# Kernel optimization log

Hardware: AMD Instinct MI355X
Metric: run time of the kernel (lower is better)

## Reference

```python
import jax, jax.numpy as jnp
import numpy as np

N = 100000
E = 800000
D = 128


def setup_inputs() -> dict:
    key = jax.random.key(0)
    k1, k2, k3, k4 = jax.random.split(key, 4)
    x = jax.random.normal(k1, (N, D), dtype=jnp.float32)
    edge_index = jax.random.randint(k2, (2, E), 0, N, dtype=jnp.int64)
    s = 1.0 / np.sqrt(D)
    W1 = jax.random.uniform(k3, (D, D), jnp.float32, -s, s)
    b1 = jnp.zeros((D,), jnp.float32)
    W2 = jax.random.uniform(k4, (D, D), jnp.float32, -s, s)
    b2 = jnp.zeros((D,), jnp.float32)
    return {"x": x, "edge_index": edge_index, "W1": W1, "b1": b1, "W2": W2, "b2": b2}


def _degree(idx, n, dtype):
    return jax.ops.segment_sum(jnp.ones(idx.shape, dtype), idx, num_segments=n)


def _graph_conv(x, row, col, W, b, residual, act):
    n = x.shape[0]
    deg_out = jnp.clip(_degree(row, n, x.dtype), 1.0)          # [N]
    x_src = x * jax.lax.rsqrt(deg_out)[:, None]                # [N, D]
    # scatter-add messages from source (row) into target (col)
    agg = jax.ops.segment_sum(x_src[row], col, num_segments=n)  # [N, D]
    out = agg @ W.T + b
    deg_in = jnp.clip(_degree(col, n, x.dtype), 1.0)
    out = out * jax.lax.rsqrt(deg_in)[:, None]
    if residual:
        out = out + x  # res_fc is Identity (in_dim == out_dim)
    if act:
        out = jax.nn.relu(out)
    return out


def reference(x, edge_index, W1, b1, W2, b2):
    row, col = edge_index[0], edge_index[1]
    # layer 1: relu + residual; layer 2 (last, encoding=False): no act, no residual
    h = _graph_conv(x, row, col, W1, b1, residual=True, act=True)
    h = _graph_conv(h, row, col, W2, b2, residual=False, act=False)
    return h
```

## Files before the change

kernel.cpp:

```cpp
#include <hip/hip_runtime.h>


#define NN 100000
#define EE 800000
#define DD 128
#define NB1 98
#define NTILE (NN / 16)

#define CC 64
#define CH (EE / CC)
#define HALF 50000
#define HWORDS 12500
#define NWORDS 25000

typedef __attribute__((ext_vector_type(8))) short short8;
typedef __attribute__((ext_vector_type(4))) float floatx4;

__device__ inline float bf2f(unsigned int u16) {
    union { unsigned int i; float f; } c;
    c.i = u16 << 16;
    return c.f;
}
__device__ inline ushort f2bf(float f) {
    union { float f; unsigned int i; } c;
    c.f = f;
    unsigned int u = c.i;
    return (ushort)((u + 0x7fffu + ((u >> 16) & 1u)) >> 16);
}

__global__ __launch_bounds__(512) void count_kernel(const int* __restrict__ row,
                                                    const int* __restrict__ col,
                                                    unsigned int* __restrict__ partial_out,
                                                    unsigned int* __restrict__ partial_in,
                                                    unsigned char* __restrict__ off_u8) {
    __shared__ unsigned int h[HWORDS];
    for (int i = threadIdx.x; i < HWORDS; i += 512) h[i] = 0;
    __syncthreads();

    const int kind = blockIdx.x >> 7;
    const int r = (blockIdx.x >> 6) & 1;
    const int c = blockIdx.x & 63;
    const int* __restrict__ idx = kind ? row : col;
    const int base = c * CH;
    const int lo = r * HALF;

    for (int t = threadIdx.x; t < CH; t += 512) {
        const int e = base + t;
        const unsigned int d = (unsigned int)(idx[e] - lo);
        if (d < (unsigned int)HALF) {
            const int sh = 8 * (d & 3);
            unsigned int old = atomicAdd(&h[d >> 2], 1u << sh);
            if (kind == 0) off_u8[e] = (unsigned char)((old >> sh) & 0xffu);
        }
    }
    __syncthreads();

    unsigned int* dst = (kind ? partial_out : partial_in) + c * NWORDS + r * HWORDS;
    for (int i = threadIdx.x; i < HWORDS; i += 512) dst[i] = h[i];
}

__global__ __launch_bounds__(256) void node_kernel(const unsigned int* __restrict__ partial_out,
                                                   const unsigned int* __restrict__ partial_in,
                                                   int* __restrict__ cnt_total,
                                                   unsigned int* __restrict__ xoff,
                                                   float* __restrict__ dinv_out,
                                                   float* __restrict__ dinv_in) {
    const int w = blockIdx.x * 256 + threadIdx.x;
    if (w >= NWORDS) return;
    unsigned int prefix = 0;
    unsigned int tot_out = 0;
#pragma unroll
    for (int c = 0; c < CC; ++c) {
        unsigned int v = partial_in[c * NWORDS + w];
        xoff[c * NWORDS + w] = prefix;
        prefix += v;
        tot_out += partial_out[c * NWORDS + w];
    }
    int4 ct;
    float4 fi, fo;
#pragma unroll
    for (int j = 0; j < 4; ++j) {
        int din  = (int)((prefix  >> (8 * j)) & 0xffu);
        int dout = (int)((tot_out >> (8 * j)) & 0xffu);
        ((int*)&ct)[j]   = din;
        ((float*)&fi)[j] = rsqrtf((float)max(din, 1));
        ((float*)&fo)[j] = rsqrtf((float)max(dout, 1));
    }
    ((int4*)cnt_total)[w] = ct;
    ((float4*)dinv_in)[w] = fi;
    ((float4*)dinv_out)[w] = fo;
}

__global__ __launch_bounds__(256) void scan1_kernel(const int* __restrict__ cnt,
                                                    int* __restrict__ excl,
                                                    int* __restrict__ bsums) {
    __shared__ int tmp[256];
    const int t = threadIdx.x;
    const int base = blockIdx.x * 1024 + t * 4;
    int a[4];
#pragma unroll
    for (int q = 0; q < 4; ++q) a[q] = (base + q < NN) ? cnt[base + q] : 0;
    int s = a[0] + a[1] + a[2] + a[3];
    tmp[t] = s;
    __syncthreads();
    for (int off = 1; off < 256; off <<= 1) {
        int v = 0;
        if (t >= off) v = tmp[t - off];
        __syncthreads();
        tmp[t] += v;
        __syncthreads();
    }
    int excl_s = tmp[t] - s;
    if (t == 255) bsums[blockIdx.x] = tmp[t];
    int run = excl_s;
#pragma unroll
    for (int q = 0; q < 4; ++q) {
        if (base + q < NN) excl[base + q] = run;
        run += a[q];
    }
}

__global__ __launch_bounds__(256) void scan2_kernel(int* __restrict__ bsums, int nb) {
    __shared__ int tmp[256];
    const int t = threadIdx.x;
    int s = (t < nb) ? bsums[t] : 0;
    tmp[t] = s;
    __syncthreads();
    for (int off = 1; off < 256; off <<= 1) {
        int v = 0;
        if (t >= off) v = tmp[t - off];
        __syncthreads();
        tmp[t] += v;
        __syncthreads();
    }
    if (t < nb) bsums[t] = tmp[t] - s;
}

__global__ __launch_bounds__(256) void scan3_kernel(const int* __restrict__ excl,
                                                    const int* __restrict__ bsums,
                                                    int* __restrict__ row_start) {
    int i = blockIdx.x * 256 + threadIdx.x;
    if (i < NN) row_start[i] = excl[i] + bsums[i >> 10];
}

__global__ __launch_bounds__(256) void fill_kernel(const int* __restrict__ row,
                                                   const int* __restrict__ col,
                                                   const int* __restrict__ row_start,
                                                   const unsigned char* __restrict__ xoff_u8,
                                                   const unsigned char* __restrict__ off_u8,
                                                   int* __restrict__ srcs) {
    int e = blockIdx.x * 256 + threadIdx.x;
    if (e < EE) {
        const int cl = col[e];
        const int c = e / CH;
        const int pos = row_start[cl] + (int)xoff_u8[(size_t)c * NN + cl] + (int)off_u8[e];
        srcs[pos] = row[e];
    }
}

__global__ __launch_bounds__(256) void prescale_kernel(const float* __restrict__ x,
                                                       const float* __restrict__ dinv_out,
                                                       ushort* __restrict__ xb) {
    int idx = blockIdx.x * 256 + threadIdx.x;
    if (idx >= NN * 32) return;
    int n = idx >> 5;
    float s = dinv_out[n];
    float4 v = ((const float4*)x)[idx];
    ushort4 o;
    o.x = f2bf(v.x * s);
    o.y = f2bf(v.y * s);
    o.z = f2bf(v.z * s);
    o.w = f2bf(v.w * s);
    ((ushort4*)xb)[idx] = o;
}

__global__ __launch_bounds__(256) void gather_kernel(const ushort* __restrict__ src,
                                                     const int* __restrict__ row_start,
                                                     const int* __restrict__ srcs,
                                                     ushort* __restrict__ agg) {
    const int node = blockIdx.x * 16 + (threadIdx.x >> 4);
    const int lane = threadIdx.x & 15;
    if (node >= NN) return;
    int p = row_start[node];
    const int end = (node + 1 < NN) ? row_start[node + 1] : EE;
    float a0 = 0.f, a1 = 0.f, a2 = 0.f, a3 = 0.f;
    float a4 = 0.f, a5 = 0.f, a6 = 0.f, a7 = 0.f;

#define ACCUM(V)                                     \
    do {                                             \
        a0 += bf2f((V).x & 0xffffu);                 \
        a1 += bf2f((V).x >> 16);                     \
        a2 += bf2f((V).y & 0xffffu);                 \
        a3 += bf2f((V).y >> 16);                     \
        a4 += bf2f((V).z & 0xffffu);                 \
        a5 += bf2f((V).z >> 16);                     \
        a6 += bf2f((V).w & 0xffffu);                 \
        a7 += bf2f((V).w >> 16);                     \
    } while (0)

    for (; p + 3 < end; p += 4) {
        int s0 = srcs[p];
        int s1 = srcs[p + 1];
        int s2 = srcs[p + 2];
        int s3 = srcs[p + 3];
        uint4 v0 = ((const uint4*)(src + (size_t)s0 * DD))[lane];
        uint4 v1 = ((const uint4*)(src + (size_t)s1 * DD))[lane];
        uint4 v2 = ((const uint4*)(src + (size_t)s2 * DD))[lane];
        uint4 v3 = ((const uint4*)(src + (size_t)s3 * DD))[lane];
        ACCUM(v0); ACCUM(v1); ACCUM(v2); ACCUM(v3);
    }
    for (; p < end; ++p) {
        int s0 = srcs[p];
        uint4 v0 = ((const uint4*)(src + (size_t)s0 * DD))[lane];
        ACCUM(v0);
    }
#undef ACCUM

    uint4 o;
    o.x = (unsigned int)f2bf(a0) | ((unsigned int)f2bf(a1) << 16);
    o.y = (unsigned int)f2bf(a2) | ((unsigned int)f2bf(a3) << 16);
    o.z = (unsigned int)f2bf(a4) | ((unsigned int)f2bf(a5) << 16);
    o.w = (unsigned int)f2bf(a6) | ((unsigned int)f2bf(a7) << 16);
    ((uint4*)(agg + (size_t)node * DD))[lane] = o;
}

template <bool L1>
__global__ __launch_bounds__(256) void gemm_ep(const ushort* __restrict__ agg,
                                               const float* __restrict__ W,
                                               const float* __restrict__ bias,
                                               const float* __restrict__ dinv_in,
                                               const float* __restrict__ dinv_out,
                                               const float* __restrict__ x,
                                               ushort* __restrict__ hs,
                                               float* __restrict__ out) {
    __shared__ ushort Ws[128 * 136];
    {
        int j = threadIdx.x >> 1;
        int k0 = (threadIdx.x & 1) * 64;
        const float4* wp = (const float4*)(W + (size_t)j * DD + k0);
        ushort* dst = Ws + j * 136 + k0;
#pragma unroll
        for (int q = 0; q < 16; ++q) {
            float4 v = wp[q];
            ushort4 o;
            o.x = f2bf(v.x); o.y = f2bf(v.y); o.z = f2bf(v.z); o.w = f2bf(v.w);
            *(ushort4*)(dst + q * 4) = o;
        }
    }
    __syncthreads();

    const int wave = threadIdx.x >> 6;
    const int lane = threadIdx.x & 63;
    const int tile = blockIdx.x * 4 + wave;
    if (tile >= NTILE) return;
    const int mi = lane & 15;
    const int quad = lane >> 4;
    const int m0 = tile * 16;

    floatx4 acc[8];
#pragma unroll
    for (int t = 0; t < 8; ++t) acc[t] = (floatx4){0.f, 0.f, 0.f, 0.f};

    const ushort* ap = agg + (size_t)(m0 + mi) * DD + quad * 8;
#pragma unroll
    for (int s = 0; s < 4; ++s) {
        short8 a = *(const short8*)(ap + s * 32);
#pragma unroll
        for (int t = 0; t < 8; ++t) {
            short8 b = *(const short8*)(Ws + (t * 16 + mi) * 136 + s * 32 + quad * 8);
            acc[t] = __builtin_amdgcn_mfma_f32_16x16x32_bf16(a, b, acc[t], 0, 0, 0);
        }
    }

    float dv[4], dov[4];
#pragma unroll
    for (int i = 0; i < 4; ++i) {
        int r = m0 + quad * 4 + i;
        dv[i] = dinv_in[r];
        if (L1) dov[i] = dinv_out[r];
    }
#pragma unroll
    for (int t = 0; t < 8; ++t) {
        int c = t * 16 + mi;
        float bv = bias[c];
#pragma unroll
        for (int i = 0; i < 4; ++i) {
            int r = m0 + quad * 4 + i;
            float o = (acc[t][i] + bv) * dv[i];
            if (L1) {
                o += x[(size_t)r * DD + c];
                o = fmaxf(o, 0.f);
                hs[(size_t)r * DD + c] = f2bf(o * dov[i]);
            } else {
                out[(size_t)r * DD + c] = o;
            }
        }
    }
}

extern "C" void kernel_launch(void* const* d_in, const int* in_sizes, int n_in,
                              void* d_out, int out_size, void* d_ws, size_t ws_size,
                              hipStream_t stream) {
    const float* x  = (const float*)d_in[0];
    const int*   ei = (const int*)d_in[1];
    const float* W1 = (const float*)d_in[2];
    const float* b1 = (const float*)d_in[3];
    const float* W2 = (const float*)d_in[4];
    const float* b2 = (const float*)d_in[5];
    float* out = (float*)d_out;

    const int* row = ei;
    const int* col = ei + EE;

    ushort* agg     = (ushort*)d_ws;
    ushort* xb      = agg + (size_t)NN * DD;
    float* dinv_out = (float*)(xb + (size_t)NN * DD);
    float* dinv_in  = dinv_out + NN;
    int*   cnt      = (int*)(dinv_in + NN);
    int*   excl     = cnt + NN;
    int*   row_st   = excl + NN;
    int*   srcs     = row_st + NN;
    int*   bsums    = srcs + EE;

    unsigned char* off_u8      = (unsigned char*)agg;
    unsigned int*  partial_in  = (unsigned int*)(off_u8 + EE);
    unsigned int*  partial_out = partial_in + CC * NWORDS;
    unsigned int*  xoff        = partial_out + CC * NWORDS;

    count_kernel<<<256, 512, 0, stream>>>(row, col, partial_out, partial_in, off_u8);
    node_kernel<<<(NWORDS + 255) / 256, 256, 0, stream>>>(partial_out, partial_in, cnt, xoff,
                                                          dinv_out, dinv_in);
    scan1_kernel<<<NB1, 256, 0, stream>>>(cnt, excl, bsums);
    scan2_kernel<<<1, 256, 0, stream>>>(bsums, NB1);
    scan3_kernel<<<(NN + 255) / 256, 256, 0, stream>>>(excl, bsums, row_st);
    fill_kernel<<<(EE + 255) / 256, 256, 0, stream>>>(row, col, row_st,
                                                      (const unsigned char*)xoff, off_u8, srcs);

    prescale_kernel<<<(NN * 32 + 255) / 256, 256, 0, stream>>>(x, dinv_out, xb);
    gather_kernel<<<(NN + 15) / 16, 256, 0, stream>>>(xb, row_st, srcs, agg);
    gemm_ep<true><<<(NTILE + 3) / 4, 256, 0, stream>>>(agg, W1, b1, dinv_in, dinv_out, x,
                                                       xb, nullptr);

    gather_kernel<<<(NN + 15) / 16, 256, 0, stream>>>(xb, row_st, srcs, agg);
    gemm_ep<false><<<(NTILE + 3) / 4, 256, 0, stream>>>(agg, W2, b2, dinv_in, nullptr, nullptr,
                                                        nullptr, out);
}
```

Before: 280.9 us.

## Fuse neighbor gather with MFMA GEMM epilogue via shared-memory tile

Each block now gathers 64 nodes' aggregated bf16 rows into an LDS tile and runs the 16x16x32 bf16 MFMA GEMM plus epilogue directly from it. This removes the global round-trip of the agg buffer between separate gather and GEMM kernels. The weights are converted to bf16 once by a new wconv kernel and read from global/L1 instead of being staged into shared memory per block. Layer 1 writes its hidden output into the scratch buffer so layer 2 can gather from it while xb is no longer overwritten. The trade-off is a larger per-block working set, and B-fragment loads that now go to global memory rather than LDS.

```diff
diff --git a/kernel.cpp b/kernel.cpp
--- a/kernel.cpp
+++ b/kernel.cpp
@@ -6,12 +6,15 @@
 #define DD 128
 #define NB1 98
 #define NTILE (NN / 16)
+#define NBLK ((NN + 63) / 64)
 
 #define CC 64
 #define CH (EE / CC)
 #define HALF 50000
 #define HWORDS 12500
 #define NWORDS 25000
+
+#define ASTR 144
 
 typedef __attribute__((ext_vector_type(8))) short short8;
 typedef __attribute__((ext_vector_type(4))) float floatx4;
@@ -174,17 +177,45 @@
     ((ushort4*)xb)[idx] = o;
 }
 
-__global__ __launch_bounds__(256) void gather_kernel(const ushort* __restrict__ src,
-                                                     const int* __restrict__ row_start,
-                                                     const int* __restrict__ srcs,
-                                                     ushort* __restrict__ agg) {
-    const int node = blockIdx.x * 16 + (threadIdx.x >> 4);
-    const int lane = threadIdx.x & 15;
-    if (node >= NN) return;
-    int p = row_start[node];
-    const int end = (node + 1 < NN) ? row_start[node + 1] : EE;
-    float a0 = 0.f, a1 = 0.f, a2 = 0.f, a3 = 0.f;
-    float a4 = 0.f, a5 = 0.f, a6 = 0.f, a7 = 0.f;
+__global__ __launch_bounds__(256) void wconv_kernel(const float* __restrict__ W1,
+                                                    const float* __restrict__ W2,
+                                                    ushort* __restrict__ wb1,
+                                                    ushort* __restrict__ wb2) {
+    int i = blockIdx.x * 256 + threadIdx.x;
+    const float* W = (i < 4096) ? W1 : W2;
+    ushort* wb = (i < 4096) ? wb1 : wb2;
+    int j = i & 4095;
+    if (i >= 8192) return;
+    float4 v = ((const float4*)W)[j];
+    ushort4 o;
+    o.x = f2bf(v.x); o.y = f2bf(v.y); o.z = f2bf(v.z); o.w = f2bf(v.w);
+    ((ushort4*)wb)[j] = o;
+}
+
+template <bool L1>
+__global__ __launch_bounds__(256) void gather_gemm(const ushort* __restrict__ src,
+                                                   const int* __restrict__ row_start,
+                                                   const int* __restrict__ srcs,
+                                                   const ushort* __restrict__ wb,
+                                                   const float* __restrict__ bias,
+                                                   const float* __restrict__ dinv_in,
+                                                   const float* __restrict__ dinv_out,
+                                                   const float* __restrict__ x,
+                                                   ushort* __restrict__ hs,
+                                                   float* __restrict__ out) {
+    __shared__ ushort At[64 * ASTR];
+
+    const int lane16 = threadIdx.x & 15;
+
+#pragma unroll
+    for (int pass = 0; pass < 4; ++pass) {
+        const int nl = pass * 16 + (threadIdx.x >> 4);
+        const int node = blockIdx.x * 64 + nl;
+        if (node < NN) {
+            int p = row_start[node];
+            const int end = (node + 1 < NN) ? row_start[node + 1] : EE;
+            float a0 = 0.f, a1 = 0.f, a2 = 0.f, a3 = 0.f;
+            float a4 = 0.f, a5 = 0.f, a6 = 0.f, a7 = 0.f;
 
 #define ACCUM(V)                                     \
     do {                                             \
@@ -198,53 +229,30 @@
         a7 += bf2f((V).w >> 16);                     \
     } while (0)
 
-    for (; p + 3 < end; p += 4) {
-        int s0 = srcs[p];
-        int s1 = srcs[p + 1];
-        int s2 = srcs[p + 2];
-        int s3 = srcs[p + 3];
-        uint4 v0 = ((const uint4*)(src + (size_t)s0 * DD))[lane];
-        uint4 v1 = ((const uint4*)(src + (size_t)s1 * DD))[lane];
-        uint4 v2 = ((const uint4*)(src + (size_t)s2 * DD))[lane];
-        uint4 v3 = ((const uint4*)(src + (size_t)s3 * DD))[lane];
-        ACCUM(v0); ACCUM(v1); ACCUM(v2); ACCUM(v3);
-    }
-    for (; p < end; ++p) {
-        int s0 = srcs[p];
-        uint4 v0 = ((const uint4*)(src + (size_t)s0 * DD))[lane];
-        ACCUM(v0);
-    }
+            for (; p + 3 < end; p += 4) {
+                int s0 = srcs[p];
+                int s1 = srcs[p + 1];
+                int s2 = srcs[p + 2];
+                int s3 = srcs[p + 3];
+                uint4 v0 = ((const uint4*)(src + (size_t)s0 * DD))[lane16];
+                uint4 v1 = ((const uint4*)(src + (size_t)s1 * DD))[lane16];
+                uint4 v2 = ((const uint4*)(src + (size_t)s2 * DD))[lane16];
+                uint4 v3 = ((const uint4*)(src + (size_t)s3 * DD))[lane16];
+                ACCUM(v0); ACCUM(v1); ACCUM(v2); ACCUM(v3);
+            }
+            for (; p < end; ++p) {
+                int s0 = srcs[p];
+                uint4 v0 = ((const uint4*)(src + (size_t)s0 * DD))[lane16];
+                ACCUM(v0);
+            }
 #undef ACCUM
 
-    uint4 o;
-    o.x = (unsigned int)f2bf(a0) | ((unsigned int)f2bf(a1) << 16);
-    o.y = (unsigned int)f2bf(a2) | ((unsigned int)f2bf(a3) << 16);
-    o.z = (unsigned int)f2bf(a4) | ((unsigned int)f2bf(a5) << 16);
-    o.w = (unsigned int)f2bf(a6) | ((unsigned int)f2bf(a7) << 16);
-    ((uint4*)(agg + (size_t)node * DD))[lane] = o;
-}
-
-template <bool L1>
-__global__ __launch_bounds__(256) void gemm_ep(const ushort* __restrict__ agg,
-                                               const float* __restrict__ W,
-                                               const float* __restrict__ bias,
-                                               const float* __restrict__ dinv_in,
-                                               const float* __restrict__ dinv_out,
-                                               const float* __restrict__ x,
-                                               ushort* __restrict__ hs,
-                                               float* __restrict__ out) {
-    __shared__ ushort Ws[128 * 136];
-    {
-        int j = threadIdx.x >> 1;
-        int k0 = (threadIdx.x & 1) * 64;
-        const float4* wp = (const float4*)(W + (size_t)j * DD + k0);
-        ushort* dst = Ws + j * 136 + k0;
-#pragma unroll
-        for (int q = 0; q < 16; ++q) {
-            float4 v = wp[q];
-            ushort4 o;
-            o.x = f2bf(v.x); o.y = f2bf(v.y); o.z = f2bf(v.z); o.w = f2bf(v.w);
-            *(ushort4*)(dst + q * 4) = o;
+            uint4 o;
+            o.x = (unsigned int)f2bf(a0) | ((unsigned int)f2bf(a1) << 16);
+            o.y = (unsigned int)f2bf(a2) | ((unsigned int)f2bf(a3) << 16);
+            o.z = (unsigned int)f2bf(a4) | ((unsigned int)f2bf(a5) << 16);
+            o.w = (unsigned int)f2bf(a6) | ((unsigned int)f2bf(a7) << 16);
+            *(uint4*)(At + nl * ASTR + lane16 * 8) = o;
         }
     }
     __syncthreads();
@@ -261,14 +269,18 @@
 #pragma unroll
     for (int t = 0; t < 8; ++t) acc[t] = (floatx4){0.f, 0.f, 0.f, 0.f};
 
-    const ushort* ap = agg + (size_t)(m0 + mi) * DD + quad * 8;
+    const ushort* ap = At + (wave * 16 + mi) * ASTR + quad * 8;
+    short8 afr[4];
+#pragma unroll
+    for (int s = 0; s < 4; ++s) afr[s] = *(const short8*)(ap + s * 32);
+
+    const ushort* bp = wb + (size_t)mi * DD + quad * 8;
 #pragma unroll
     for (int s = 0; s < 4; ++s) {
-        short8 a = *(const short8*)(ap + s * 32);
 #pragma unroll
         for (int t = 0; t < 8; ++t) {
-            short8 b = *(const short8*)(Ws + (t * 16 + mi) * 136 + s * 32 + quad * 8);
-            acc[t] = __builtin_amdgcn_mfma_f32_16x16x32_bf16(a, b, acc[t], 0, 0, 0);
+            short8 b = *(const short8*)(bp + (size_t)t * 16 * DD + s * 32);
+            acc[t] = __builtin_amdgcn_mfma_f32_16x16x32_bf16(afr[s], b, acc[t], 0, 0, 0);
         }
     }
 
@@ -312,8 +324,8 @@
     const int* row = ei;
     const int* col = ei + EE;
 
-    ushort* agg     = (ushort*)d_ws;
-    ushort* xb      = agg + (size_t)NN * DD;
+    ushort* scratch = (ushort*)d_ws;
+    ushort* xb      = scratch + (size_t)NN * DD;
     float* dinv_out = (float*)(xb + (size_t)NN * DD);
     float* dinv_in  = dinv_out + NN;
     int*   cnt      = (int*)(dinv_in + NN);
@@ -321,12 +333,15 @@
     int*   row_st   = excl + NN;
     int*   srcs     = row_st + NN;
     int*   bsums    = srcs + EE;
-
-    unsigned char* off_u8      = (unsigned char*)agg;
+    ushort* wb1     = (ushort*)(bsums + 256);
+    ushort* wb2     = wb1 + DD * DD;
+
+    unsigned char* off_u8      = (unsigned char*)scratch;
     unsigned int*  partial_in  = (unsigned int*)(off_u8 + EE);
     unsigned int*  partial_out = partial_in + CC * NWORDS;
     unsigned int*  xoff        = partial_out + CC * NWORDS;
 
+    wconv_kernel<<<32, 256, 0, stream>>>(W1, W2, wb1, wb2);
     count_kernel<<<256, 512, 0, stream>>>(row, col, partial_out, partial_in, off_u8);
     node_kernel<<<(NWORDS + 255) / 256, 256, 0, stream>>>(partial_out, partial_in, cnt, xoff,
                                                           dinv_out, dinv_in);
@@ -337,11 +352,9 @@
                                                       (const unsigned char*)xoff, off_u8, srcs);
 
     prescale_kernel<<<(NN * 32 + 255) / 256, 256, 0, stream>>>(x, dinv_out, xb);
-    gather_kernel<<<(NN + 15) / 16, 256, 0, stream>>>(xb, row_st, srcs, agg);
-    gemm_ep<true><<<(NTILE + 3) / 4, 256, 0, stream>>>(agg, W1, b1, dinv_in, dinv_out, x,
-                                                       xb, nullptr);
-
-    gather_kernel<<<(NN + 15) / 16, 256, 0, stream>>>(xb, row_st, srcs, agg);
-    gemm_ep<false><<<(NTILE + 3) / 4, 256, 0, stream>>>(agg, W2, b2, dinv_in, nullptr, nullptr,
-                                                        nullptr, out);
-}
+    gather_gemm<true><<<NBLK, 256, 0, stream>>>(xb, row_st, srcs, wb1, b1, dinv_in, dinv_out,
+                                                x, (ushort*)scratch, nullptr);
+
+    gather_gemm<false><<<NBLK, 256, 0, stream>>>((ushort*)scratch, row_st, srcs, wb2, b2,
+                                                 dinv_in, nullptr, nullptr, nullptr, out);
+}
```

Result: slower. 301.3 us (+7.3%).
